# Optimization experiments

Hardware: AMD Instinct MI355X
Metric: run time of the kernel (lower is better)

Reference implementation:

```python
import jax, jax.numpy as jnp
import numpy as np

N_NODES = 50000
N_EDGES = 500000
IN_F, HID, EMB = 128, 256, 128

def setup_inputs() -> dict:
    key = jax.random.key(0)
    ks = jax.random.split(key, 9)
    x = jax.random.normal(ks[0], (N_NODES, IN_F), dtype=jnp.float32)
    src = jax.random.randint(ks[1], (N_EDGES,), 0, N_NODES, dtype=jnp.int32)
    dst = jax.random.randint(ks[2], (N_EDGES,), 0, N_NODES, dtype=jnp.int32)
    def lin(k, fan_in, fan_out):
        bound = 1.0 / np.sqrt(fan_in)
        kw, kb = jax.random.split(k)
        W = jax.random.uniform(kw, (fan_in, fan_out), minval=-bound, maxval=bound, dtype=jnp.float32)
        b = jax.random.uniform(kb, (fan_out,), minval=-bound, maxval=bound, dtype=jnp.float32)
        return W, b
    W1, b1 = lin(ks[3], IN_F, HID)
    W2, b2 = lin(ks[4], HID, HID)
    W3, b3 = lin(ks[5], HID, EMB)
    return {"x": x, "src": src, "dst": dst, "W1": W1, "b1": b1,
            "W2": W2, "b2": b2, "W3": W3, "b3": b3}

def _gcn_layer(h, src, dst, W, b):
    # sum messages from src nodes into dst nodes, then linear
    agg = jax.ops.segment_sum(h[src], dst, num_segments=N_NODES)  # [N, F]
    return agg @ W + b

def reference(x, src, dst, W1, b1, W2, b2, W3, b3):
    h = jax.nn.relu(_gcn_layer(x, src, dst, W1, b1))
    h = jax.nn.relu(_gcn_layer(h, src, dst, W2, b2))
    h = _gcn_layer(h, src, dst, W3, b3)
    # dgl.mean_nodes on a single graph: mean of relu(h) over all nodes -> [EMB]
    return jnp.mean(jax.nn.relu(h), axis=0)
```

## Files before the change

### kernel.cpp

```cpp
#include <hip/hip_runtime.h>

#define N_NODES 50000
#define N_EDGES 500000

typedef __attribute__((ext_vector_type(8))) short short8;
typedef __attribute__((ext_vector_type(8))) unsigned short ushort8v;
typedef __attribute__((ext_vector_type(4))) float floatx4;
typedef __attribute__((ext_vector_type(4))) unsigned int uint4v;

__device__ inline float bf2f(unsigned short u) {
    unsigned int x = ((unsigned int)u) << 16;
    return __builtin_bit_cast(float, x);
}
__device__ inline unsigned short f2bf(float f) {
    unsigned int x = __builtin_bit_cast(unsigned int, f);
    x += 0x7fff + ((x >> 16) & 1);
    return (unsigned short)(x >> 16);
}

__device__ inline void accum16B(float2* a, ushort8v rv) {
    uint4v u = __builtin_bit_cast(uint4v, rv);
    #pragma unroll
    for (int p = 0; p < 4; p++) {
        float lo = __builtin_bit_cast(float, u[p] << 16);
        float hi = __builtin_bit_cast(float, u[p] & 0xFFFF0000u);
        a[p].x += lo;
        a[p].y += hi;
    }
}


__global__ void scan_block_kernel(const int* __restrict__ deg, int* __restrict__ partial,
                                  int* __restrict__ bsum, int n) {
    __shared__ int s[256];
    int i = blockIdx.x * 256 + threadIdx.x;
    int v = (i < n) ? deg[i] : 0;
    s[threadIdx.x] = v;
    __syncthreads();
    #pragma unroll
    for (int d = 1; d < 256; d <<= 1) {
        int t = (threadIdx.x >= d) ? s[threadIdx.x - d] : 0;
        __syncthreads();
        s[threadIdx.x] += t;
        __syncthreads();
    }
    if (i < n) partial[i] = s[threadIdx.x];
    if (threadIdx.x == 255) bsum[blockIdx.x] = s[255];
}

__global__ __launch_bounds__(256) void finalize_kernel(const int* __restrict__ partial,
                                                       const int* __restrict__ bsum,
                                                       int* __restrict__ cur,
                                                       int* __restrict__ off, int n) {
    __shared__ int sr[256];
    int t = threadIdx.x;
    sr[t] = (t < blockIdx.x) ? bsum[t] : 0;
    __syncthreads();
    #pragma unroll
    for (int d = 128; d > 0; d >>= 1) {
        if (t < d) sr[t] += sr[t + d];
        __syncthreads();
    }
    int base = sr[0];
    int i = blockIdx.x * 256 + t;
    if (i == 0) off[0] = 0;
    if (i < n) {
        int incl = base + partial[i];
        off[i + 1] = incl;
        cur[i] = incl - cur[i];
    }
}

__global__ void fill_kernel(const int* __restrict__ src, const int* __restrict__ dst,
                            int* __restrict__ cur, int* __restrict__ csr, int nE) {
    int e = blockIdx.x * 256 + threadIdx.x;
    if (e < nE) {
        int p = atomicAdd(&cur[dst[e]], 1);
        csr[p] = src[e];
    }
}


__global__ __launch_bounds__(256) void histprep_kernel(const int* __restrict__ dst,
                                                       int* __restrict__ deg,
                                                       const float* __restrict__ W1,
                                                       const float* __restrict__ W2,
                                                       const float* __restrict__ W3,
                                                       const float* __restrict__ x,
                                                       unsigned short* __restrict__ Wt1,
                                                       unsigned short* __restrict__ Wt2,
                                                       unsigned short* __restrict__ Wt3,
                                                       unsigned short* __restrict__ xb) {
    int idx = blockIdx.x * 256 + threadIdx.x;
    if (idx < N_EDGES) { atomicAdd(&deg[dst[idx]], 1); return; }
    idx -= N_EDGES;
    if (idx < 32768) {
        int k = idx >> 8, n = idx & 255;
        Wt1[n * 128 + k] = f2bf(W1[idx]);
    } else if (idx < 98304) {
        int i = idx - 32768;
        int k = i >> 8, n = i & 255;
        Wt2[n * 256 + k] = f2bf(W2[i]);
    } else if (idx < 131072) {
        int i = idx - 98304;
        int k = i >> 7, n = i & 127;
        Wt3[n * 256 + k] = f2bf(W3[i]);
    } else {
        int i = (idx - 131072) * 4;
        if (i < N_NODES * 128) {
            float4 v = *(const float4*)(x + i);
            ushort4 o;
            o.x = f2bf(v.x); o.y = f2bf(v.y); o.z = f2bf(v.z); o.w = f2bf(v.w);
            *(ushort4*)(xb + i) = o;
        }
    }
}


__global__ __launch_bounds__(256) void agg256_kernel(const unsigned short* __restrict__ h,
                                                     const int* __restrict__ off,
                                                     const int* __restrict__ csr,
                                                     unsigned short* __restrict__ outp) {
    int wave = threadIdx.x >> 6, lane = threadIdx.x & 63;
    int node = blockIdx.x * 4 + wave;
    int half = lane >> 5;
    int f0 = (lane & 31) * 8;
    int s = __builtin_amdgcn_readfirstlane(off[node]);
    int e = __builtin_amdgcn_readfirstlane(off[node + 1]);
    float2 a[4];
    #pragma unroll
    for (int p = 0; p < 4; p++) a[p] = make_float2(0.f, 0.f);
    int i = s;
    for (; i + 8 <= e; i += 8) {
        ushort8v r[4];
        #pragma unroll
        for (int j = 0; j < 4; j++) {
            int i0 = csr[i + 2 * j];
            int i1 = csr[i + 2 * j + 1];
            int id = half ? i1 : i0;
            r[j] = *(const ushort8v*)(h + (size_t)id * 256 + f0);
        }
        #pragma unroll
        for (int j = 0; j < 4; j++) accum16B(a, r[j]);
    }
    int rem = e - i;
    if (rem > 0) {
        int nr = (rem + 1) >> 1;
        ushort8v r[4];
        #pragma unroll
        for (int j = 0; j < 4; j++) {
            if (j < nr) {
                int b0 = i + 2 * j, b1 = b0 + 1;
                int i0 = csr[b0];
                int i1 = csr[b1 < e ? b1 : e - 1];
                int id = half ? i1 : i0;
                r[j] = *(const ushort8v*)(h + (size_t)id * 256 + f0);
            }
        }
        #pragma unroll
        for (int j = 0; j < 4; j++) {
            if (j < nr && (i + 2 * j + half) < e) accum16B(a, r[j]);
        }
    }
    #pragma unroll
    for (int p = 0; p < 4; p++) {
        a[p].x += __shfl_xor(a[p].x, 32, 64);
        a[p].y += __shfl_xor(a[p].y, 32, 64);
    }
    if (half == 0) {
        ushort8v o;
        #pragma unroll
        for (int p = 0; p < 4; p++) { o[2 * p] = f2bf(a[p].x); o[2 * p + 1] = f2bf(a[p].y); }
        *(ushort8v*)(outp + (size_t)node * 256 + f0) = o;
    }
}


__device__ inline void agg128_body(const unsigned short* __restrict__ h,
                                   const int* __restrict__ off,
                                   const int* __restrict__ csr,
                                   int node, int quad, int f0, float2* a) {
    int s = __builtin_amdgcn_readfirstlane(off[node]);
    int e = __builtin_amdgcn_readfirstlane(off[node + 1]);
    int i = s;
    for (; i + 8 <= e; i += 8) {
        ushort8v r[2];
        #pragma unroll
        for (int j = 0; j < 2; j++) {
            int base = i + 4 * j;
            int i0 = csr[base], i1 = csr[base + 1], i2 = csr[base + 2], i3 = csr[base + 3];
            int id = quad == 0 ? i0 : quad == 1 ? i1 : quad == 2 ? i2 : i3;
            r[j] = *(const ushort8v*)(h + (size_t)id * 128 + f0);
        }
        #pragma unroll
        for (int j = 0; j < 2; j++) accum16B(a, r[j]);
    }
    int rem = e - i;
    if (rem > 0) {
        int nr = (rem + 3) >> 2;
        ushort8v r[2];
        #pragma unroll
        for (int j = 0; j < 2; j++) {
            if (j < nr) {
                int base = i + 4 * j;
                int c0 = base;
                int c1 = base + 1 < e ? base + 1 : e - 1;
                int c2 = base + 2 < e ? base + 2 : e - 1;
                int c3 = base + 3 < e ? base + 3 : e - 1;
                int i0 = csr[c0], i1 = csr[c1], i2 = csr[c2], i3 = csr[c3];
                int id = quad == 0 ? i0 : quad == 1 ? i1 : quad == 2 ? i2 : i3;
                r[j] = *(const ushort8v*)(h + (size_t)id * 128 + f0);
            }
        }
        #pragma unroll
        for (int j = 0; j < 2; j++) {
            if (j < nr && (i + 4 * j + quad) < e) accum16B(a, r[j]);
        }
    }
    #pragma unroll
    for (int p = 0; p < 4; p++) {
        a[p].x += __shfl_xor(a[p].x, 16, 64);
        a[p].y += __shfl_xor(a[p].y, 16, 64);
        a[p].x += __shfl_xor(a[p].x, 32, 64);
        a[p].y += __shfl_xor(a[p].y, 32, 64);
    }
}

__global__ __launch_bounds__(256) void agg128_kernel(const unsigned short* __restrict__ h,
                                                     const int* __restrict__ off,
                                                     const int* __restrict__ csr,
                                                     unsigned short* __restrict__ outp) {
    int wave = threadIdx.x >> 6, lane = threadIdx.x & 63;
    int node = blockIdx.x * 4 + wave;
    int quad = lane >> 4;
    int f0 = (lane & 15) * 8;
    float2 a[4];
    #pragma unroll
    for (int p = 0; p < 4; p++) a[p] = make_float2(0.f, 0.f);
    agg128_body(h, off, csr, node, quad, f0, a);
    if (quad == 0) {
        ushort8v o;
        #pragma unroll
        for (int p = 0; p < 4; p++) { o[2 * p] = f2bf(a[p].x); o[2 * p + 1] = f2bf(a[p].y); }
        *(ushort8v*)(outp + (size_t)node * 128 + f0) = o;
    }
}


__global__ __launch_bounds__(256) void agg3_mean_kernel(const unsigned short* __restrict__ t,
                                                        const int* __restrict__ off,
                                                        const int* __restrict__ csr,
                                                        const float* __restrict__ b3,
                                                        float* __restrict__ partial) {
    __shared__ float sm[4 * 128];
    int wave = threadIdx.x >> 6, lane = threadIdx.x & 63;
    int node = blockIdx.x * 4 + wave;
    int quad = lane >> 4;
    int f0 = (lane & 15) * 8;
    float2 a[4];
    #pragma unroll
    for (int p = 0; p < 4; p++) a[p] = make_float2(0.f, 0.f);
    agg128_body(t, off, csr, node, quad, f0, a);
    if (quad == 0) {
        #pragma unroll
        for (int p = 0; p < 4; p++) {
            sm[wave * 128 + f0 + 2 * p]     = fmaxf(a[p].x + b3[f0 + 2 * p], 0.f);
            sm[wave * 128 + f0 + 2 * p + 1] = fmaxf(a[p].y + b3[f0 + 2 * p + 1], 0.f);
        }
    }
    __syncthreads();
    if (threadIdx.x < 128) {
        int f = threadIdx.x;
        float p = sm[f] + sm[128 + f] + sm[256 + f] + sm[384 + f];
        partial[(size_t)blockIdx.x * 128 + f] = p;
    }
}

__global__ __launch_bounds__(256) void mean_reduce_kernel(const float* __restrict__ partial,
                                                          float* __restrict__ outp, int nRows) {
    __shared__ float s[256];
    int f = threadIdx.x & 127, half = threadIdx.x >> 7;
    int chunk = (nRows + gridDim.x - 1) / gridDim.x;
    int r0 = blockIdx.x * chunk;
    int r1 = r0 + chunk < nRows ? r0 + chunk : nRows;
    float acc = 0.f;
    for (int r = r0 + half; r < r1; r += 2) acc += partial[(size_t)r * 128 + f];
    s[threadIdx.x] = acc;
    __syncthreads();
    if (half == 0) atomicAdd(&outp[f], (s[f] + s[f + 128]) * (1.0f / N_NODES));
}


template<typename T> __device__ inline void storeC(T* p, float v);
template<> __device__ inline void storeC<float>(float* p, float v) { *p = v; }
template<> __device__ inline void storeC<unsigned short>(unsigned short* p, float v) { *p = f2bf(v); }

template<int BN, typename OUT_T>
__global__ __launch_bounds__(2 * BN) void gemm_bf16_kernel(const unsigned short* __restrict__ A,
                                                           const unsigned short* __restrict__ Bt,
                                                           const float* __restrict__ bias,
                                                           OUT_T* __restrict__ C,
                                                           int M, int K, int N, int doRelu) {
    constexpr int BM = 128, BK = 32, LDA = BK + 8;
    constexpr int T = 2 * BN;
    __shared__ unsigned short As[BM * LDA];
    __shared__ unsigned short Bs[BN * LDA];
    int tid = threadIdx.x;
    int m0 = blockIdx.y * BM, n0 = blockIdx.x * BN;
    int wave = tid >> 6, lane = tid & 63;
    int wm = wave & 1, wn = wave >> 1;
    int mlane = lane & 15, kgrp = lane >> 4;

    floatx4 acc[4][4];
    #pragma unroll
    for (int i = 0; i < 4; i++)
        #pragma unroll
        for (int j = 0; j < 4; j++) acc[i][j] = (floatx4){0.f, 0.f, 0.f, 0.f};

    for (int k0 = 0; k0 < K; k0 += BK) {
        #pragma unroll
        for (int c = tid; c < 512; c += T) {
            int r = c >> 2, cb = (c & 3) * 8;
            int rg = m0 + r;
            short8 v;
            if (rg < M) v = *(const short8*)(A + (size_t)rg * K + k0 + cb);
            else        v = (short8){0, 0, 0, 0, 0, 0, 0, 0};
            *(short8*)&As[r * LDA + cb] = v;
        }
        #pragma unroll
        for (int c = tid; c < BN * 4; c += T) {
            int r = c >> 2, cb = (c & 3) * 8;
            short8 w = *(const short8*)(Bt + (size_t)(n0 + r) * K + k0 + cb);
            *(short8*)&Bs[r * LDA + cb] = w;
        }
        __syncthreads();
        short8 af[4], bfr[4];
        #pragma unroll
        for (int mt = 0; mt < 4; mt++)
            af[mt] = *(const short8*)&As[(wm * 64 + mt * 16 + mlane) * LDA + kgrp * 8];
        #pragma unroll
        for (int nt = 0; nt < 4; nt++)
            bfr[nt] = *(const short8*)&Bs[(wn * 64 + nt * 16 + mlane) * LDA + kgrp * 8];
        #pragma unroll
        for (int mt = 0; mt < 4; mt++)
            #pragma unroll
            for (int nt = 0; nt < 4; nt++)
                acc[mt][nt] = __builtin_amdgcn_mfma_f32_16x16x32_bf16(af[mt], bfr[nt],
                                                                      acc[mt][nt], 0, 0, 0);
        __syncthreads();
    }
    #pragma unroll
    for (int mt = 0; mt < 4; mt++) {
        #pragma unroll
        for (int nt = 0; nt < 4; nt++) {
            int col = n0 + wn * 64 + nt * 16 + mlane;
            float bv = bias ? bias[col] : 0.f;
            #pragma unroll
            for (int r = 0; r < 4; r++) {
                int row = m0 + wm * 64 + mt * 16 + kgrp * 4 + r;
                if (row < M) {
                    float v = acc[mt][nt][r] + bv;
                    if (doRelu) v = fmaxf(v, 0.f);
                    storeC(C + (size_t)row * N + col, v);
                }
            }
        }
    }
}


extern "C" void kernel_launch(void* const* d_in, const int* in_sizes, int n_in,
                              void* d_out, int out_size, void* d_ws, size_t ws_size,
                              hipStream_t stream) {
    const float* x   = (const float*)d_in[0];
    const int*   src = (const int*)d_in[1];
    const int*   dst = (const int*)d_in[2];
    const float* W1 = (const float*)d_in[3];
    const float* b1 = (const float*)d_in[4];
    const float* W2 = (const float*)d_in[5];
    const float* b2 = (const float*)d_in[6];
    const float* W3 = (const float*)d_in[7];
    const float* b3 = (const float*)d_in[8];
    float* out = (float*)d_out;

    char* ws = (char*)d_ws;
    size_t o = 0;
    auto alloc = [&](size_t bytes) -> char* {
        char* p = ws + o;
        o = (o + bytes + 255) & ~(size_t)255;
        return p;
    };
    int* off     = (int*)alloc((size_t)(N_NODES + 1) * 4);
    int* cur     = (int*)alloc((size_t)N_NODES * 4);
    int* csr     = (int*)alloc((size_t)N_EDGES * 4);
    int* partial = (int*)alloc((size_t)N_NODES * 4);
    int* bsum    = (int*)alloc(256 * 4);
    unsigned short* Wt1 = (unsigned short*)alloc((size_t)128 * 256 * 2);
    unsigned short* Wt2 = (unsigned short*)alloc((size_t)256 * 256 * 2);
    unsigned short* Wt3 = (unsigned short*)alloc((size_t)256 * 128 * 2);
    char* R1 = alloc((size_t)N_NODES * 256 * 2);
    char* R2 = alloc((size_t)N_NODES * 256 * 2);
    char* R3 = alloc((size_t)N_NODES * 256 * 2);

    unsigned short* xb    = (unsigned short*)R1;
    unsigned short* aggX  = (unsigned short*)R2;
    unsigned short* h1    = (unsigned short*)R3;
    unsigned short* agg2o = (unsigned short*)R1;
    unsigned short* h2    = (unsigned short*)R2;
    unsigned short* t     = (unsigned short*)R3;
    float*          pmean = (float*)R1;

    const int nb = (N_NODES + 255) / 256;

    hipMemsetAsync(cur, 0, (size_t)N_NODES * 4, stream);
    const int hpThreads = N_EDGES + 131072 + N_NODES * 128 / 4;
    histprep_kernel<<<(hpThreads + 255) / 256, 256, 0, stream>>>(dst, cur, W1, W2, W3, x,
                                                                 Wt1, Wt2, Wt3, xb);
    scan_block_kernel<<<nb, 256, 0, stream>>>(cur, partial, bsum, N_NODES);
    finalize_kernel<<<nb, 256, 0, stream>>>(partial, bsum, cur, off, N_NODES);
    fill_kernel<<<(N_EDGES + 255) / 256, 256, 0, stream>>>(src, dst, cur, csr, N_EDGES);

    const int mb = (N_NODES + 127) / 128;

    agg128_kernel<<<N_NODES / 4, 256, 0, stream>>>(xb, off, csr, aggX);
    gemm_bf16_kernel<256, unsigned short><<<dim3(1, mb), 512, 0, stream>>>(aggX, Wt1, b1, h1,
                                                                           N_NODES, 128, 256, 1);
    agg256_kernel<<<N_NODES / 4, 256, 0, stream>>>(h1, off, csr, agg2o);
    gemm_bf16_kernel<256, unsigned short><<<dim3(1, mb), 512, 0, stream>>>(agg2o, Wt2, b2, h2,
                                                                           N_NODES, 256, 256, 1);
    gemm_bf16_kernel<128, unsigned short><<<dim3(1, mb), 256, 0, stream>>>(h2, Wt3, nullptr, t,
                                                                           N_NODES, 256, 128, 0);
    agg3_mean_kernel<<<N_NODES / 4, 256, 0, stream>>>(t, off, csr, b3, pmean);

    hipMemsetAsync(out, 0, 128 * 4, stream);
    mean_reduce_kernel<<<128, 256, 0, stream>>>(pmean, out, N_NODES / 4);
}
```

Measured before the change: 301.3 us.

## Fuse CSR build and weight prep into one cooperative grid-synced kernel

Replaces the memsets plus histogram/prep, block scan, finalize and fill kernels with a single cooperative kernel of 512 blocks that uses grid.sync between phases. It also folds the zeroing of the output into that kernel. This removes several launches and memset overheads from the preprocessing chain. The trade-off is that the grid is fixed at 512 blocks, so grid-stride loops replace the wide one-shot launches and four grid-wide barriers are added. The scan needs 196 blocks, which fits under 512.

```diff
diff --git a/kernel.cpp b/kernel.cpp
--- a/kernel.cpp
+++ b/kernel.cpp
@@ -1,4 +1,7 @@
 #include <hip/hip_runtime.h>
+#include <hip/hip_cooperative_groups.h>
+
+namespace cg = cooperative_groups;
 
 #define N_NODES 50000
 #define N_EDGES 500000
@@ -30,59 +33,8 @@
 }
 
 
-__global__ void scan_block_kernel(const int* __restrict__ deg, int* __restrict__ partial,
-                                  int* __restrict__ bsum, int n) {
-    __shared__ int s[256];
-    int i = blockIdx.x * 256 + threadIdx.x;
-    int v = (i < n) ? deg[i] : 0;
-    s[threadIdx.x] = v;
-    __syncthreads();
-    #pragma unroll
-    for (int d = 1; d < 256; d <<= 1) {
-        int t = (threadIdx.x >= d) ? s[threadIdx.x - d] : 0;
-        __syncthreads();
-        s[threadIdx.x] += t;
-        __syncthreads();
-    }
-    if (i < n) partial[i] = s[threadIdx.x];
-    if (threadIdx.x == 255) bsum[blockIdx.x] = s[255];
-}
-
-__global__ __launch_bounds__(256) void finalize_kernel(const int* __restrict__ partial,
-                                                       const int* __restrict__ bsum,
-                                                       int* __restrict__ cur,
-                                                       int* __restrict__ off, int n) {
-    __shared__ int sr[256];
-    int t = threadIdx.x;
-    sr[t] = (t < blockIdx.x) ? bsum[t] : 0;
-    __syncthreads();
-    #pragma unroll
-    for (int d = 128; d > 0; d >>= 1) {
-        if (t < d) sr[t] += sr[t + d];
-        __syncthreads();
-    }
-    int base = sr[0];
-    int i = blockIdx.x * 256 + t;
-    if (i == 0) off[0] = 0;
-    if (i < n) {
-        int incl = base + partial[i];
-        off[i + 1] = incl;
-        cur[i] = incl - cur[i];
-    }
-}
-
-__global__ void fill_kernel(const int* __restrict__ src, const int* __restrict__ dst,
-                            int* __restrict__ cur, int* __restrict__ csr, int nE) {
-    int e = blockIdx.x * 256 + threadIdx.x;
-    if (e < nE) {
-        int p = atomicAdd(&cur[dst[e]], 1);
-        csr[p] = src[e];
-    }
-}
-
-
-__global__ __launch_bounds__(256) void histprep_kernel(const int* __restrict__ dst,
-                                                       int* __restrict__ deg,
+__global__ __launch_bounds__(256) void csr_coop_kernel(const int* __restrict__ src,
+                                                       const int* __restrict__ dst,
                                                        const float* __restrict__ W1,
                                                        const float* __restrict__ W2,
                                                        const float* __restrict__ W3,
@@ -90,29 +42,85 @@
                                                        unsigned short* __restrict__ Wt1,
                                                        unsigned short* __restrict__ Wt2,
                                                        unsigned short* __restrict__ Wt3,
-                                                       unsigned short* __restrict__ xb) {
-    int idx = blockIdx.x * 256 + threadIdx.x;
-    if (idx < N_EDGES) { atomicAdd(&deg[dst[idx]], 1); return; }
-    idx -= N_EDGES;
-    if (idx < 32768) {
-        int k = idx >> 8, n = idx & 255;
-        Wt1[n * 128 + k] = f2bf(W1[idx]);
-    } else if (idx < 98304) {
-        int i = idx - 32768;
+                                                       unsigned short* __restrict__ xb,
+                                                       int* __restrict__ cur,
+                                                       int* __restrict__ partial,
+                                                       int* __restrict__ bsum,
+                                                       int* __restrict__ off,
+                                                       int* __restrict__ csrIdx,
+                                                       float* __restrict__ out) {
+    cg::grid_group grid = cg::this_grid();
+    const int gsize = gridDim.x * 256;
+    const int gtid = blockIdx.x * 256 + threadIdx.x;
+    const int nb = (N_NODES + 255) / 256;
+
+    for (int i = gtid; i < N_NODES; i += gsize) cur[i] = 0;
+    if (gtid < 128) out[gtid] = 0.f;
+    for (int i = gtid; i < 32768; i += gsize) {
+        int k = i >> 8, n = i & 255;
+        Wt1[n * 128 + k] = f2bf(W1[i]);
+    }
+    for (int i = gtid; i < 65536; i += gsize) {
         int k = i >> 8, n = i & 255;
         Wt2[n * 256 + k] = f2bf(W2[i]);
-    } else if (idx < 131072) {
-        int i = idx - 98304;
+    }
+    for (int i = gtid; i < 32768; i += gsize) {
         int k = i >> 7, n = i & 127;
         Wt3[n * 256 + k] = f2bf(W3[i]);
-    } else {
-        int i = (idx - 131072) * 4;
-        if (i < N_NODES * 128) {
-            float4 v = *(const float4*)(x + i);
-            ushort4 o;
-            o.x = f2bf(v.x); o.y = f2bf(v.y); o.z = f2bf(v.z); o.w = f2bf(v.w);
-            *(ushort4*)(xb + i) = o;
-        }
+    }
+    for (int i = gtid; i < N_NODES * 128 / 4; i += gsize) {
+        float4 v = *(const float4*)(x + i * 4);
+        ushort4 o;
+        o.x = f2bf(v.x); o.y = f2bf(v.y); o.z = f2bf(v.z); o.w = f2bf(v.w);
+        *(ushort4*)(xb + i * 4) = o;
+    }
+    grid.sync();
+
+    for (int e = gtid; e < N_EDGES; e += gsize) atomicAdd(&cur[dst[e]], 1);
+    grid.sync();
+
+    __shared__ int s[256];
+    __shared__ int sr[256];
+    if (blockIdx.x < nb) {
+        int i = blockIdx.x * 256 + threadIdx.x;
+        int v = (i < N_NODES) ? cur[i] : 0;
+        s[threadIdx.x] = v;
+        __syncthreads();
+        #pragma unroll
+        for (int d = 1; d < 256; d <<= 1) {
+            int t = (threadIdx.x >= d) ? s[threadIdx.x - d] : 0;
+            __syncthreads();
+            s[threadIdx.x] += t;
+            __syncthreads();
+        }
+        if (i < N_NODES) partial[i] = s[threadIdx.x];
+        if (threadIdx.x == 255) bsum[blockIdx.x] = s[255];
+    }
+    grid.sync();
+
+    if (blockIdx.x < nb) {
+        int t = threadIdx.x;
+        sr[t] = (t < blockIdx.x) ? bsum[t] : 0;
+        __syncthreads();
+        #pragma unroll
+        for (int d = 128; d > 0; d >>= 1) {
+            if (t < d) sr[t] += sr[t + d];
+            __syncthreads();
+        }
+        int base = sr[0];
+        int i = blockIdx.x * 256 + t;
+        if (i == 0) off[0] = 0;
+        if (i < N_NODES) {
+            int incl = base + partial[i];
+            off[i + 1] = incl;
+            cur[i] = incl - cur[i];
+        }
+    }
+    grid.sync();
+
+    for (int e = gtid; e < N_EDGES; e += gsize) {
+        int p = atomicAdd(&cur[dst[e]], 1);
+        csrIdx[p] = src[e];
     }
 }
 
@@ -203,11 +211,10 @@
         for (int j = 0; j < 2; j++) {
             if (j < nr) {
                 int base = i + 4 * j;
-                int c0 = base;
                 int c1 = base + 1 < e ? base + 1 : e - 1;
                 int c2 = base + 2 < e ? base + 2 : e - 1;
                 int c3 = base + 3 < e ? base + 3 : e - 1;
-                int i0 = csr[c0], i1 = csr[c1], i2 = csr[c2], i3 = csr[c3];
+                int i0 = csr[base], i1 = csr[c1], i2 = csr[c2], i3 = csr[c3];
                 int id = quad == 0 ? i0 : quad == 1 ? i1 : quad == 2 ? i2 : i3;
                 r[j] = *(const ushort8v*)(h + (size_t)id * 128 + f0);
             }
@@ -392,7 +399,7 @@
     };
     int* off     = (int*)alloc((size_t)(N_NODES + 1) * 4);
     int* cur     = (int*)alloc((size_t)N_NODES * 4);
-    int* csr     = (int*)alloc((size_t)N_EDGES * 4);
+    int* csrIdx  = (int*)alloc((size_t)N_EDGES * 4);
     int* partial = (int*)alloc((size_t)N_NODES * 4);
     int* bsum    = (int*)alloc(256 * 4);
     unsigned short* Wt1 = (unsigned short*)alloc((size_t)128 * 256 * 2);
@@ -410,28 +417,27 @@
     unsigned short* t     = (unsigned short*)R3;
     float*          pmean = (float*)R1;
 
-    const int nb = (N_NODES + 255) / 256;
-
-    hipMemsetAsync(cur, 0, (size_t)N_NODES * 4, stream);
-    const int hpThreads = N_EDGES + 131072 + N_NODES * 128 / 4;
-    histprep_kernel<<<(hpThreads + 255) / 256, 256, 0, stream>>>(dst, cur, W1, W2, W3, x,
-                                                                 Wt1, Wt2, Wt3, xb);
-    scan_block_kernel<<<nb, 256, 0, stream>>>(cur, partial, bsum, N_NODES);
-    finalize_kernel<<<nb, 256, 0, stream>>>(partial, bsum, cur, off, N_NODES);
-    fill_kernel<<<(N_EDGES + 255) / 256, 256, 0, stream>>>(src, dst, cur, csr, N_EDGES);
+    {
+        void* coopArgs[] = {
+            (void*)&src, (void*)&dst, (void*)&W1, (void*)&W2, (void*)&W3, (void*)&x,
+            (void*)&Wt1, (void*)&Wt2, (void*)&Wt3, (void*)&xb,
+            (void*)&cur, (void*)&partial, (void*)&bsum, (void*)&off, (void*)&csrIdx,
+            (void*)&out
+        };
+        hipLaunchCooperativeKernel((void*)csr_coop_kernel, dim3(512), dim3(256),
+                                   coopArgs, 0, stream);
+    }
 
     const int mb = (N_NODES + 127) / 128;
 
-    agg128_kernel<<<N_NODES / 4, 256, 0, stream>>>(xb, off, csr, aggX);
+    agg128_kernel<<<N_NODES / 4, 256, 0, stream>>>(xb, off, csrIdx, aggX);
     gemm_bf16_kernel<256, unsigned short><<<dim3(1, mb), 512, 0, stream>>>(aggX, Wt1, b1, h1,
                                                                            N_NODES, 128, 256, 1);
-    agg256_kernel<<<N_NODES / 4, 256, 0, stream>>>(h1, off, csr, agg2o);
+    agg256_kernel<<<N_NODES / 4, 256, 0, stream>>>(h1, off, csrIdx, agg2o);
     gemm_bf16_kernel<256, unsigned short><<<dim3(1, mb), 512, 0, stream>>>(agg2o, Wt2, b2, h2,
                                                                            N_NODES, 256, 256, 1);
     gemm_bf16_kernel<128, unsigned short><<<dim3(1, mb), 256, 0, stream>>>(h2, Wt3, nullptr, t,
                                                                            N_NODES, 256, 128, 0);
-    agg3_mean_kernel<<<N_NODES / 4, 256, 0, stream>>>(t, off, csr, b3, pmean);
-
-    hipMemsetAsync(out, 0, 128 * 4, stream);
+    agg3_mean_kernel<<<N_NODES / 4, 256, 0, stream>>>(t, off, csrIdx, b3, pmean);
     mean_reduce_kernel<<<128, 256, 0, stream>>>(pmean, out, N_NODES / 4);
 }
```

New measurement: 543.4 us. 80.4% more time.
